# Optimization experiments

Hardware: AMD Instinct MI355X
Metric: run time of the kernel (lower is better)

The kernel has to match this reference:

```python
import jax, jax.numpy as jnp
import numpy as np

B, N, C, H, P = 4, 8192, 256, 4, 64  # batch, tokens(=input_size), hidden, heads, proj_size
D = C // H


def setup_inputs() -> dict:
    key = jax.random.key(0)
    ks = jax.random.split(key, 12)
    s = 1.0 / np.sqrt(C)
    inp = {
        "x": jax.random.normal(ks[0], (B, N, C), jnp.float32),
        "q": jax.random.normal(ks[1], (B, N, C), jnp.float32),
        "Wq": jax.random.normal(ks[2], (C, C), jnp.float32) * s,
        "Wk": jax.random.normal(ks[3], (C, C), jnp.float32) * s,
        "Wv_ca": jax.random.normal(ks[4], (C, C), jnp.float32) * s,
        "Wv_sa": jax.random.normal(ks[5], (C, C), jnp.float32) * s,
        "E_w": jax.random.normal(ks[6], (P, N), jnp.float32) * (1.0 / np.sqrt(N)),
        "E_b": jnp.zeros((P,), jnp.float32),
        "temp": jnp.ones((H, 1, 1), jnp.float32),
        "temp2": jnp.ones((H, 1, 1), jnp.float32),
        "Wo1": jax.random.normal(ks[7], (C // 2, C), jnp.float32) * s,
        "bo1": jnp.zeros((C // 2,), jnp.float32),
        "Wo2": jax.random.normal(ks[8], (C // 2, C), jnp.float32) * s,
        "bo2": jnp.zeros((C // 2,), jnp.float32),
    }
    return inp


def _l2norm(t):
    # F.normalize(dim=-1): x / max(||x||_2, 1e-12)
    n = jnp.sqrt(jnp.sum(t * t, axis=-1, keepdims=True))
    return t / jnp.maximum(n, 1e-12)


def reference(x, q, Wq, Wk, Wv_ca, Wv_sa, E_w, E_b, temp, temp2, Wo1, bo1, Wo2, bo2):
    b, n, c = x.shape
    h, d = H, c // H

    def split(t):  # [B,N,C] -> [B,H,d,N]
        return t.reshape(b, n, h, d).transpose(0, 2, 3, 1)

    qs = split(q @ Wq.T)
    ks = split(x @ Wk.T)
    v_ca = split(x @ Wv_ca.T)
    v_sa = split(x @ Wv_sa.T)

    # Linformer-style projections E (=F) over token dim N -> P
    k_proj = jnp.einsum('bhdn,pn->bhdp', ks, E_w) + E_b   # [B,H,d,P]
    v_proj = jnp.einsum('bhdn,pn->bhdp', v_sa, E_w) + E_b  # [B,H,d,P]

    qn = _l2norm(qs)
    kn = _l2norm(ks)

    # Channel attention: [B,H,d,d]
    attn_ca = jax.nn.softmax(jnp.einsum('bhdn,bhen->bhde', qn, kn) * temp, axis=-1)
    x_ca = jnp.einsum('bhde,bhen->bhdn', attn_ca, v_ca)
    x_ca = x_ca.transpose(0, 3, 1, 2).reshape(b, n, c)

    # Spatial (projected) attention: [B,H,N,P]
    attn_sa = jax.nn.softmax(jnp.einsum('bhdn,bhdp->bhnp', qn, k_proj) * temp2, axis=-1)
    x_sa = jnp.einsum('bhnp,bhdp->bhnd', attn_sa, v_proj)
    # faithful to original permute(0,3,1,2).reshape(B,N,C)
    x_sa = x_sa.transpose(0, 3, 1, 2).reshape(b, n, c)

    x_sa = x_sa @ Wo1.T + bo1
    x_ca = x_ca @ Wo2.T + bo2
    return jnp.concatenate((x_sa, x_ca), axis=-1)
```

## Files before the change

### kernel.cpp

```cpp
#include <hip/hip_runtime.h>
#include <hip/hip_bf16.h>

#define NN 8192
#define BNC 8388608

typedef unsigned short u16;
typedef unsigned int u32;
typedef __attribute__((ext_vector_type(8))) short bf16x8;
typedef __attribute__((ext_vector_type(4))) float f32x4;
typedef __attribute__((ext_vector_type(4))) float float4v;

__device__ __forceinline__ float bf2f(u16 u) {
    union { u32 i; float f; } c; c.i = ((u32)u) << 16; return c.f;
}
__device__ __forceinline__ u16 f2bf(float f) {
    union { float f; u32 i; } c; c.f = f;
    u32 x = c.i;
    u32 r = (x + 0x7fffu + ((x >> 16) & 1u)) >> 16;
    return (u16)r;
}
__device__ __forceinline__ void gl16(const u16* g, u16* l) {
    __builtin_amdgcn_global_load_lds(
        (const __attribute__((address_space(1))) void*)g,
        (__attribute__((address_space(3))) void*)l, 16, 0, 0);
}

__global__ void fill_kernel(float* __restrict__ out, float val) {
    int base = (blockIdx.x * 256 + threadIdx.x) * 4;
    #pragma unroll
    for (int i = 0; i < 4; ++i) out[base + i] = val;
}

__global__ void zeroconv_kernel(const float* __restrict__ q, const float* __restrict__ x,
                                const float* __restrict__ Wq, const float* __restrict__ Wk,
                                const float* __restrict__ Wo1, const float* __restrict__ Ew,
                                u16* __restrict__ qb, u16* __restrict__ xb,
                                u16* __restrict__ Wqb, u16* __restrict__ Wkb,
                                u16* __restrict__ Wo1b, u16* __restrict__ Ewb,
                                float* __restrict__ zbase) {
    if (blockIdx.x >= 8528) {
        int i = (blockIdx.x - 8528) * 256 + threadIdx.x;
        if (i < 67584) zbase[i] = 0.f;
        return;
    }
    size_t e = ((size_t)blockIdx.x * 256 + threadIdx.x) * 8;
    const float* src; u16* dst;
    if (e < 8388608)       { src = q   + e;              dst = qb   + e; }
    else if (e < 16777216) { src = x   + (e - 8388608);  dst = xb   + (e - 8388608); }
    else if (e < 16842752) { src = Wq  + (e - 16777216); dst = Wqb  + (e - 16777216); }
    else if (e < 16908288) { src = Wk  + (e - 16842752); dst = Wkb  + (e - 16842752); }
    else if (e < 16941056) { src = Wo1 + (e - 16908288); dst = Wo1b + (e - 16908288); }
    else                   { src = Ew  + (e - 16941056); dst = Ewb  + (e - 16941056); }
    float4v f0 = *(const float4v*)src, f1 = *(const float4v*)(src + 4);
    bf16x8 v;
    #pragma unroll
    for (int j = 0; j < 4; ++j) {
        v[j] = (short)f2bf(f0[j]); v[4 + j] = (short)f2bf(f1[j]);
    }
    *(bf16x8*)dst = v;
}

__global__ __launch_bounds__(256) void gemm_qkf(
    const u16* __restrict__ qb, const u16* __restrict__ xb,
    const u16* __restrict__ Wqb, const u16* __restrict__ Wkb,
    u16* __restrict__ Qb, u16* __restrict__ Kb,
    float* __restrict__ nq2, float* __restrict__ nk2)
{
    __shared__ u16 As[4096];
    __shared__ u16 Bs[4096];
    const int z = blockIdx.z;
    const u16* A = z ? xb : qb;
    const u16* Bt = z ? Wkb : Wqb;
    u16* O = z ? Kb : Qb;
    float* dstn = z ? nk2 : nq2;
    const int t = threadIdx.x, lane = t & 63, w = t >> 6;
    const int wr = w >> 1, wc = w & 1;
    const int fr = lane & 15, fk = (lane >> 4) * 8, r0 = (lane >> 4) * 4;
    const int m0 = blockIdx.x * 128, n0 = blockIdx.y * 128;
    const int b = m0 >> 13;
    const int row0 = t >> 2, k80 = (t & 3) * 8;
    const int row1 = (256 + t) >> 2, k81 = ((256 + t) & 3) * 8;

    f32x4 acc[4][4];
    #pragma unroll
    for (int i = 0; i < 4; ++i)
        #pragma unroll
        for (int j = 0; j < 4; ++j) acc[i][j] = (f32x4){0.f, 0.f, 0.f, 0.f};

    for (int kt = 0; kt < 8; ++kt) {
        const int k0 = kt * 32;
        gl16(A  + (size_t)(m0 + row0) * 256 + k0 + k80, &As[t * 8]);
        gl16(A  + (size_t)(m0 + row1) * 256 + k0 + k81, &As[(256 + t) * 8]);
        gl16(Bt + (size_t)(n0 + row0) * 256 + k0 + k80, &Bs[t * 8]);
        gl16(Bt + (size_t)(n0 + row1) * 256 + k0 + k81, &Bs[(256 + t) * 8]);
        __syncthreads();
        bf16x8 a[4], b[4];
        #pragma unroll
        for (int fm = 0; fm < 4; ++fm)
            a[fm] = *(const bf16x8*)&As[(wr * 64 + fm * 16 + fr) * 32 + fk];
        #pragma unroll
        for (int fn = 0; fn < 4; ++fn)
            b[fn] = *(const bf16x8*)&Bs[(wc * 64 + fn * 16 + fr) * 32 + fk];
        #pragma unroll
        for (int fm = 0; fm < 4; ++fm)
            #pragma unroll
            for (int fn = 0; fn < 4; ++fn)
                acc[fm][fn] = __builtin_amdgcn_mfma_f32_16x16x32_bf16(
                    a[fm], b[fn], acc[fm][fn], 0, 0, 0);
        __syncthreads();
    }

    #pragma unroll
    for (int fn = 0; fn < 4; ++fn) {
        int gcol = n0 + wc * 64 + fn * 16 + fr;
        float s = 0.f;
        #pragma unroll
        for (int fm = 0; fm < 4; ++fm) {
            #pragma unroll
            for (int r = 0; r < 4; ++r) {
                size_t grow = (size_t)(m0 + wr * 64 + fm * 16 + r0 + r);
                float v = acc[fm][fn][r];
                O[grow * 256 + gcol] = f2bf(v);
                s += v * v;
            }
        }
        s += __shfl_xor(s, 16);
        s += __shfl_xor(s, 32);
        if (lane < 16) atomicAdd(&dstn[b * 256 + gcol], s);
    }
}

__global__ __launch_bounds__(256) void xecalog_kernel(
    const u16* __restrict__ xb, const u16* __restrict__ Ewb, float* __restrict__ xE,
    const u16* __restrict__ Qb, const u16* __restrict__ Kb, float* __restrict__ cpart)
{
    __shared__ u16 smA[64][136];
    __shared__ u16 smB[64][136];
    const int t = threadIdx.x, lane = t & 63, w = t >> 6;
    const int fr = lane & 15, fk = (lane >> 4) * 8, r0 = (lane >> 4) * 4;

    f32x4 acc[4][4];
    #pragma unroll
    for (int i = 0; i < 4; ++i)
        #pragma unroll
        for (int j = 0; j < 4; ++j) acc[i][j] = (f32x4){0.f, 0.f, 0.f, 0.f};

    if (blockIdx.x < 128) {
        const int bkq = blockIdx.x >> 3, nc = blockIdx.x & 7;
        const int b = bkq >> 2, kq = bkq & 3;
        for (int it = 0; it < 8; ++it) {
            const int n0 = nc * 1024 + it * 128;
            #pragma unroll
            for (int i = 0; i < 4; ++i) {
                int c = i * 256 + t, tok = c >> 3, kl = (c & 7) * 8;
                const int sw = tok ^ ((kl >> 3) << 3);
                bf16x8 v = *(const bf16x8*)(xb + ((size_t)b * NN + n0 + tok) * 256 + kq * 64 + kl);
                #pragma unroll
                for (int j = 0; j < 8; ++j) smA[kl + j][sw] = (u16)v[j];
            }
            #pragma unroll
            for (int i = 0; i < 4; ++i) {
                int c = i * 256 + t, p = c >> 4, tk8 = (c & 15) * 8;
                *(bf16x8*)&smB[p][tk8] = *(const bf16x8*)(Ewb + (size_t)p * NN + n0 + tk8);
            }
            __syncthreads();
            bf16x8 a[4], bb[4];
            #pragma unroll
            for (int fm = 0; fm < 4; ++fm) {
                int row = fm * 16 + fr;
                a[fm] = *(const bf16x8*)&smA[row][(w * 32 + fk) ^ (((row >> 3) & 7) << 3)];
            }
            #pragma unroll
            for (int fn = 0; fn < 4; ++fn)
                bb[fn] = *(const bf16x8*)&smB[fn * 16 + fr][w * 32 + fk];
            #pragma unroll
            for (int fm = 0; fm < 4; ++fm)
                #pragma unroll
                for (int fn = 0; fn < 4; ++fn)
                    acc[fm][fn] = __builtin_amdgcn_mfma_f32_16x16x32_bf16(
                        a[fm], bb[fn], acc[fm][fn], 0, 0, 0);
            __syncthreads();
        }
        float* Cred = (float*)&smA[0][0];
        for (int ph = 0; ph < 4; ++ph) {
            if (w == ph) {
                #pragma unroll
                for (int fm = 0; fm < 4; ++fm)
                    #pragma unroll
                    for (int fn = 0; fn < 4; ++fn)
                        #pragma unroll
                        for (int r = 0; r < 4; ++r) {
                            int idx = (fm * 16 + r0 + r) * 64 + fn * 16 + fr;
                            if (ph == 0) Cred[idx] = acc[fm][fn][r];
                            else         Cred[idx] += acc[fm][fn][r];
                        }
            }
            __syncthreads();
        }
        float* dst = xE + (size_t)(b * 256 + kq * 64) * 64;
        #pragma unroll
        for (int i = 0; i < 16; ++i) atomicAdd(&dst[i * 256 + t], Cred[i * 256 + t]);
    } else {
        const int bx = blockIdx.x - 128;
        const int bh = bx >> 3, nc = bx & 7;
        const int b = bh >> 2, h = bh & 3;
        for (int it = 0; it < 8; ++it) {
            const int n0 = nc * 1024 + it * 128;
            #pragma unroll
            for (int i = 0; i < 4; ++i) {
                int c = i * 256 + t, tok = c >> 3, ch8 = (c & 7) * 8;
                const int sw = tok ^ ((ch8 >> 3) << 3);
                size_t g = ((size_t)b * NN + n0 + tok) * 256 + h * 64 + ch8;
                bf16x8 vq = *(const bf16x8*)(Qb + g);
                bf16x8 vk = *(const bf16x8*)(Kb + g);
                #pragma unroll
                for (int j = 0; j < 8; ++j) {
                    smA[ch8 + j][sw] = (u16)vq[j];
                    smB[ch8 + j][sw] = (u16)vk[j];
                }
            }
            __syncthreads();
            bf16x8 a[4], bb[4];
            #pragma unroll
            for (int fm = 0; fm < 4; ++fm) {
                int row = fm * 16 + fr;
                a[fm] = *(const bf16x8*)&smA[row][(w * 32 + fk) ^ (((row >> 3) & 7) << 3)];
            }
            #pragma unroll
            for (int fn = 0; fn < 4; ++fn) {
                int row = fn * 16 + fr;
                bb[fn] = *(const bf16x8*)&smB[row][(w * 32 + fk) ^ (((row >> 3) & 7) << 3)];
            }
            #pragma unroll
            for (int fm = 0; fm < 4; ++fm)
                #pragma unroll
                for (int fn = 0; fn < 4; ++fn)
                    acc[fm][fn] = __builtin_amdgcn_mfma_f32_16x16x32_bf16(
                        a[fm], bb[fn], acc[fm][fn], 0, 0, 0);
            __syncthreads();
        }
        float* Cred = (float*)&smA[0][0];
        for (int ph = 0; ph < 4; ++ph) {
            if (w == ph) {
                #pragma unroll
                for (int fm = 0; fm < 4; ++fm)
                    #pragma unroll
                    for (int fn = 0; fn < 4; ++fn)
                        #pragma unroll
                        for (int r = 0; r < 4; ++r) {
                            int idx = (fm * 16 + r0 + r) * 64 + fn * 16 + fr;
                            if (ph == 0) Cred[idx] = acc[fm][fn][r];
                            else         Cred[idx] += acc[fm][fn][r];
                        }
            }
            __syncthreads();
        }
        float* dst = cpart + (size_t)nc * 65536 + (size_t)bh * 4096;
        #pragma unroll
        for (int i = 0; i < 16; ++i) dst[i * 256 + t] = Cred[i * 256 + t];
    }
}

__global__ void smkv_kernel(const float* __restrict__ cpart, const float* __restrict__ nq2,
                            const float* __restrict__ nk2, const float* __restrict__ temp,
                            float* __restrict__ caprob,
                            const float* __restrict__ Wk, const float* __restrict__ Wvsa,
                            const float* __restrict__ xE, const float* __restrict__ Eb,
                            float* __restrict__ kp, float* __restrict__ vp) {
    if (blockIdx.x < 1024) {
        const int row = blockIdx.x;
        const int b = row >> 8, c = row & 255, h = c >> 6;
        const int e = threadIdx.x;
        const int i = row * 64 + e;
        float lg = cpart[i];
        #pragma unroll
        for (int nc = 1; nc < 8; ++nc) lg += cpart[(size_t)nc * 65536 + i];
        float nq = fmaxf(sqrtf(nq2[row]), 1e-12f);
        float nk = fmaxf(sqrtf(nk2[b * 256 + h * 64 + e]), 1e-12f);
        float v = lg / (nq * nk) * temp[h];
        __shared__ float red[64];
        red[e] = v; __syncthreads();
        for (int s = 32; s; s >>= 1) { if (e < s) red[e] = fmaxf(red[e], red[e + s]); __syncthreads(); }
        float m = red[0]; __syncthreads();
        float ex = __expf(v - m);
        red[e] = ex; __syncthreads();
        for (int s = 32; s; s >>= 1) { if (e < s) red[e] += red[e + s]; __syncthreads(); }
        caprob[i] = ex / red[0];
    } else {
        const int idx = blockIdx.x - 1024;
        const int z = idx >> 10, bc = idx & 1023;
        const int b = bc >> 8, c = bc & 255, p = threadIdx.x;
        const float* W = z ? Wvsa : Wk;
        float* dst = z ? vp : kp;
        float s = 0.f;
        for (int k = 0; k < 256; ++k)
            s += W[c * 256 + k] * xE[(size_t)(b * 256 + k) * 64 + p];
        dst[(size_t)(b * 256 + c) * 64 + p] = s + Eb[p];
    }
}

__global__ __launch_bounds__(256) void samw_kernel(
    const u16* __restrict__ Qb, const float* __restrict__ kp,
    const float* __restrict__ vp, const float* __restrict__ nq2,
    const float* __restrict__ temp2, u16* __restrict__ xsa,
    const float* __restrict__ caprob, const float* __restrict__ Wo2,
    const float* __restrict__ Wvca, u16* __restrict__ W2effb)
{
    __shared__ char smem[49152];
    const int t = threadIdx.x;
    if (blockIdx.x >= 512) {
        float* Ml = (float*)smem;
        const int bj = blockIdx.x - 512;
        const int b = bj >> 7, j = bj & 127;
        const int h = t >> 6, e = t & 63;
        float s = 0.f;
        #pragma unroll 8
        for (int d = 0; d < 64; ++d)
            s += Wo2[j * 256 + h * 64 + d] * caprob[(size_t)(b * 256 + h * 64 + d) * 64 + e];
        Ml[t] = s;
        __syncthreads();
        float s2 = 0.f;
        for (int c = 0; c < 256; ++c) s2 += Ml[c] * Wvca[c * 256 + t];
        W2effb[(size_t)bj * 256 + t] = f2bf(s2);
        return;
    }
    u16* Qs = (u16*)smem;
    u16* KT = (u16*)(smem + 32768);
    u16* VT = (u16*)(smem + 40960);
    const int nc = blockIdx.x & 31, bh = blockIdx.x >> 5, b = bh >> 2, h = bh & 3;
    const int lane = t & 63, w = t >> 6;
    const int fr = lane & 15, fk = (lane >> 4) * 8, r0 = (lane >> 4) * 4;

    #pragma unroll
    for (int i = 0; i < 8; ++i) {
        int c = i * 256 + t, tok = c >> 3, ch8 = (c & 7) * 8;
        *(bf16x8*)&Qs[c * 8] =
            *(const bf16x8*)(Qb + ((size_t)b * NN + nc * 256 + tok) * 256 + h * 64 + ch8);
    }
    {
        const int d = t >> 2, p0 = (t & 3) * 16;
        const float rqv = 1.0f / fmaxf(sqrtf(nq2[b * 256 + h * 64 + d]), 1e-12f);
        const float t2 = temp2[h];
        const float* kr = kp + (size_t)(b * 256 + h * 64 + d) * 64 + p0;
        #pragma unroll
        for (int j = 0; j < 16; ++j)
            KT[(p0 + j) * 64 + d] = f2bf(kr[j] * rqv * t2);
    }
    {
        const float* vs = vp + (size_t)(b * 256 + h * 64) * 64;
        #pragma unroll
        for (int i = 0; i < 2; ++i) {
            int c = i * 256 + t;
            bf16x8 v;
            #pragma unroll
            for (int j = 0; j < 8; ++j) v[j] = (short)f2bf(vs[c * 8 + j]);
            *(bf16x8*)&VT[c * 8] = v;
        }
    }
    __syncthreads();

    f32x4 acc[4][4];
    #pragma unroll
    for (int i = 0; i < 4; ++i)
        #pragma unroll
        for (int j = 0; j < 4; ++j) acc[i][j] = (f32x4){0.f, 0.f, 0.f, 0.f};
    #pragma unroll
    for (int ks = 0; ks < 2; ++ks) {
        bf16x8 a[4], bb[4];
        #pragma unroll
        for (int fm = 0; fm < 4; ++fm)
            a[fm] = *(const bf16x8*)&Qs[(w * 64 + fm * 16 + fr) * 64 + ks * 32 + fk];
        #pragma unroll
        for (int fn = 0; fn < 4; ++fn)
            bb[fn] = *(const bf16x8*)&KT[(fn * 16 + fr) * 64 + ks * 32 + fk];
        #pragma unroll
        for (int fm = 0; fm < 4; ++fm)
            #pragma unroll
            for (int fn = 0; fn < 4; ++fn)
                acc[fm][fn] = __builtin_amdgcn_mfma_f32_16x16x32_bf16(
                    a[fm], bb[fn], acc[fm][fn], 0, 0, 0);
    }
    __syncthreads();

    u16* Pw = Qs + w * 4096;
    #pragma unroll
    for (int fm = 0; fm < 4; ++fm) {
        #pragma unroll
        for (int r = 0; r < 4; ++r) {
            float m = fmaxf(fmaxf(acc[fm][0][r], acc[fm][1][r]),
                            fmaxf(acc[fm][2][r], acc[fm][3][r]));
            m = fmaxf(m, __shfl_xor(m, 1));
            m = fmaxf(m, __shfl_xor(m, 2));
            m = fmaxf(m, __shfl_xor(m, 4));
            m = fmaxf(m, __shfl_xor(m, 8));
            float e0 = __expf(acc[fm][0][r] - m), e1 = __expf(acc[fm][1][r] - m);
            float e2 = __expf(acc[fm][2][r] - m), e3 = __expf(acc[fm][3][r] - m);
            float s = e0 + e1 + e2 + e3;
            s += __shfl_xor(s, 1); s += __shfl_xor(s, 2);
            s += __shfl_xor(s, 4); s += __shfl_xor(s, 8);
            float rs = 1.0f / s;
            int row = fm * 16 + r0 + r;
            Pw[row * 64 +  0 + fr] = f2bf(e0 * rs);
            Pw[row * 64 + 16 + fr] = f2bf(e1 * rs);
            Pw[row * 64 + 32 + fr] = f2bf(e2 * rs);
            Pw[row * 64 + 48 + fr] = f2bf(e3 * rs);
        }
    }

    f32x4 acc2[4][4];
    #pragma unroll
    for (int i = 0; i < 4; ++i)
        #pragma unroll
        for (int j = 0; j < 4; ++j) acc2[i][j] = (f32x4){0.f, 0.f, 0.f, 0.f};
    #pragma unroll
    for (int ks = 0; ks < 2; ++ks) {
        bf16x8 a[4], bb[4];
        #pragma unroll
        for (int fm = 0; fm < 4; ++fm)
            a[fm] = *(const bf16x8*)&Pw[(fm * 16 + fr) * 64 + ks * 32 + fk];
        #pragma unroll
        for (int fn = 0; fn < 4; ++fn)
            bb[fn] = *(const bf16x8*)&VT[(fn * 16 + fr) * 64 + ks * 32 + fk];
        #pragma unroll
        for (int fm = 0; fm < 4; ++fm)
            #pragma unroll
            for (int fn = 0; fn < 4; ++fn)
                acc2[fm][fn] = __builtin_amdgcn_mfma_f32_16x16x32_bf16(
                    a[fm], bb[fn], acc2[fm][fn], 0, 0, 0);
    }
    __syncthreads();

    u16* X2 = Qs;
    #pragma unroll
    for (int fm = 0; fm < 4; ++fm)
        #pragma unroll
        for (int fn = 0; fn < 4; ++fn)
            #pragma unroll
            for (int r = 0; r < 4; ++r)
                X2[(w * 64 + fm * 16 + r0 + r) * 64 + fn * 16 + fr] = f2bf(acc2[fm][fn][r]);
    __syncthreads();

    {
        const int d = t >> 2, cq = (t & 3) * 64;
        u16* orow = xsa + ((size_t)b * NN + d * 128 + h * 32 + nc) * 256 + cq;
        #pragma unroll
        for (int i = 0; i < 8; ++i) {
            bf16x8 v;
            #pragma unroll
            for (int j = 0; j < 8; ++j) v[j] = (short)X2[(cq + i * 8 + j) * 64 + d];
            *(bf16x8*)&orow[i * 8] = v;
        }
    }
}

__global__ __launch_bounds__(256) void outgemm(
    const u16* __restrict__ xsa, const u16* __restrict__ xb,
    const u16* __restrict__ Wo1b, const u16* __restrict__ W2effb,
    const float* __restrict__ bo1, const float* __restrict__ bo2,
    float* __restrict__ out)
{
    __shared__ u16 As[4096];
    __shared__ u16 Bs[4096];
    const int z = blockIdx.z;
    const u16* A = z ? xb : xsa;
    const u16* Bt = z ? (W2effb + (size_t)(blockIdx.x >> 6) * 128 * 256) : Wo1b;
    const float* bias = z ? bo2 : bo1;
    const int outoff = z ? 128 : 0;
    const int t = threadIdx.x, lane = t & 63, w = t >> 6;
    const int wr = w >> 1, wc = w & 1;
    const int fr = lane & 15, fk = (lane >> 4) * 8, r0 = (lane >> 4) * 4;
    const int m0 = blockIdx.x * 128;
    const int row0 = t >> 2, k80 = (t & 3) * 8;
    const int row1 = (256 + t) >> 2, k81 = ((256 + t) & 3) * 8;

    f32x4 acc[4][4];
    #pragma unroll
    for (int i = 0; i < 4; ++i)
        #pragma unroll
        for (int j = 0; j < 4; ++j) acc[i][j] = (f32x4){0.f, 0.f, 0.f, 0.f};

    for (int kt = 0; kt < 8; ++kt) {
        const int k0 = kt * 32;
        gl16(A  + (size_t)(m0 + row0) * 256 + k0 + k80, &As[t * 8]);
        gl16(A  + (size_t)(m0 + row1) * 256 + k0 + k81, &As[(256 + t) * 8]);
        gl16(Bt + (size_t)row0 * 256 + k0 + k80, &Bs[t * 8]);
        gl16(Bt + (size_t)row1 * 256 + k0 + k81, &Bs[(256 + t) * 8]);
        __syncthreads();
        bf16x8 a[4], b[4];
        #pragma unroll
        for (int fm = 0; fm < 4; ++fm)
            a[fm] = *(const bf16x8*)&As[(wr * 64 + fm * 16 + fr) * 32 + fk];
        #pragma unroll
        for (int fn = 0; fn < 4; ++fn)
            b[fn] = *(const bf16x8*)&Bs[(wc * 64 + fn * 16 + fr) * 32 + fk];
        #pragma unroll
        for (int fm = 0; fm < 4; ++fm)
            #pragma unroll
            for (int fn = 0; fn < 4; ++fn)
                acc[fm][fn] = __builtin_amdgcn_mfma_f32_16x16x32_bf16(
                    a[fm], b[fn], acc[fm][fn], 0, 0, 0);
        __syncthreads();
    }

    #pragma unroll
    for (int fm = 0; fm < 4; ++fm)
        #pragma unroll
        for (int fn = 0; fn < 4; ++fn) {
            int gcol = wc * 64 + fn * 16 + fr;
            #pragma unroll
            for (int r = 0; r < 4; ++r) {
                size_t grow = (size_t)(m0 + wr * 64 + fm * 16 + r0 + r);
                out[grow * 256 + outoff + gcol] = acc[fm][fn][r] + bias[gcol];
            }
        }
}

extern "C" void kernel_launch(void* const* d_in, const int* in_sizes, int n_in,
                              void* d_out, int out_size, void* d_ws, size_t ws_size,
                              hipStream_t stream) {
    float* out = (float*)d_out;

    static const int expect[14] = {8388608, 8388608, 65536, 65536, 65536, 65536,
                                   524288, 64, 4, 4, 32768, 128, 32768, 128};
    bool ok = (n_in == 14) && (out_size == 8388608);
    if (ok) for (int i = 0; i < 14; ++i) ok = ok && (in_sizes[i] == expect[i]);
    if (!ok) {
        fill_kernel<<<dim3(8192), 256, 0, stream>>>(out, 3000.0f);
        return;
    }
    if (ws_size < 80000000u) {
        fill_kernel<<<dim3(8192), 256, 0, stream>>>(out, 1000.0f);
        return;
    }

    const float* x    = (const float*)d_in[0];
    const float* q    = (const float*)d_in[1];
    const float* Wq   = (const float*)d_in[2];
    const float* Wk   = (const float*)d_in[3];
    const float* Wvca = (const float*)d_in[4];
    const float* Wvsa = (const float*)d_in[5];
    const float* Ew   = (const float*)d_in[6];
    const float* Eb   = (const float*)d_in[7];
    const float* temp = (const float*)d_in[8];
    const float* temp2= (const float*)d_in[9];
    const float* Wo1  = (const float*)d_in[10];
    const float* bo1  = (const float*)d_in[11];
    const float* Wo2  = (const float*)d_in[12];
    const float* bo2  = (const float*)d_in[13];

    u16* Qb   = (u16*)d_ws;
    u16* Kb   = Qb + (size_t)BNC;
    u16* qb   = Kb + (size_t)BNC;
    u16* xb   = qb + (size_t)BNC;
    u16* Wqb  = xb + (size_t)BNC;
    u16* Wkb  = Wqb + 65536;
    u16* Wo1b = Wkb + 65536;
    u16* Ewb  = Wo1b + 32768;
    u16* W2effb = Ewb + 524288;
    u16* xsa  = Kb;
    float* fs    = (float*)(W2effb + 131072);
    float* nq2   = fs;
    float* nk2   = nq2 + 1024;
    float* xE    = nk2 + 1024;
    float* kp    = xE + 65536;
    float* vp    = kp + 65536;
    float* caprob= vp + 65536;
    float* cpart = caprob + 65536;

    zeroconv_kernel<<<dim3(8792), 256, 0, stream>>>(q, x, Wq, Wk, Wo1, Ew,
                                                    qb, xb, Wqb, Wkb, Wo1b, Ewb, nq2);
    gemm_qkf<<<dim3(256, 2, 2), 256, 0, stream>>>(qb, xb, Wqb, Wkb, Qb, Kb, nq2, nk2);
    xecalog_kernel<<<dim3(256), 256, 0, stream>>>(xb, Ewb, xE, Qb, Kb, cpart);
    smkv_kernel<<<dim3(3072), 64, 0, stream>>>(cpart, nq2, nk2, temp, caprob,
                                               Wk, Wvsa, xE, Eb, kp, vp);
    samw_kernel<<<dim3(1024), 256, 0, stream>>>(Qb, kp, vp, nq2, temp2, xsa,
                                                caprob, Wo2, Wvca, W2effb);
    outgemm<<<dim3(256, 1, 2), 256, 0, stream>>>(xsa, xb, Wo1b, W2effb, bo1, bo2, out);
}
```

Before: 110.3 us.

## Enlarge GEMM block tiles to 256 rows with 512 threads, async Q load

gemm_qkf and outgemm now run 512-thread blocks that each cover 256 rows instead of 128. The idea is to load each B (weight) tile once per 256 rows and halve the number of blocks. The samw kernel now loads its Q tile with async global-to-LDS loads instead of going through registers. The visible epilogue in gemm_qkf still indexes with wr=w>>1 and wc=w&1 for 8 waves, and its per-block norm reduction may not match the new tiling, so correctness is at risk.

```diff
diff --git a/kernel.cpp b/kernel.cpp
--- a/kernel.cpp
+++ b/kernel.cpp
@@ -60,13 +60,13 @@
     *(bf16x8*)dst = v;
 }
 
-__global__ __launch_bounds__(256) void gemm_qkf(
+__global__ __launch_bounds__(512) void gemm_qkf(
     const u16* __restrict__ qb, const u16* __restrict__ xb,
     const u16* __restrict__ Wqb, const u16* __restrict__ Wkb,
     u16* __restrict__ Qb, u16* __restrict__ Kb,
     float* __restrict__ nq2, float* __restrict__ nk2)
 {
-    __shared__ u16 As[4096];
+    __shared__ u16 As[8192];
     __shared__ u16 Bs[4096];
     const int z = blockIdx.z;
     const u16* A = z ? xb : qb;
@@ -76,10 +76,10 @@
     const int t = threadIdx.x, lane = t & 63, w = t >> 6;
     const int wr = w >> 1, wc = w & 1;
     const int fr = lane & 15, fk = (lane >> 4) * 8, r0 = (lane >> 4) * 4;
-    const int m0 = blockIdx.x * 128, n0 = blockIdx.y * 128;
+    const int m0 = blockIdx.x * 256, n0 = blockIdx.y * 128;
     const int b = m0 >> 13;
-    const int row0 = t >> 2, k80 = (t & 3) * 8;
-    const int row1 = (256 + t) >> 2, k81 = ((256 + t) & 3) * 8;
+    const int rA0 = t >> 2, kA0 = (t & 3) * 8;
+    const int rA1 = (512 + t) >> 2, kA1 = ((512 + t) & 3) * 8;
 
     f32x4 acc[4][4];
     #pragma unroll
@@ -89,24 +89,23 @@
 
     for (int kt = 0; kt < 8; ++kt) {
         const int k0 = kt * 32;
-        gl16(A  + (size_t)(m0 + row0) * 256 + k0 + k80, &As[t * 8]);
-        gl16(A  + (size_t)(m0 + row1) * 256 + k0 + k81, &As[(256 + t) * 8]);
-        gl16(Bt + (size_t)(n0 + row0) * 256 + k0 + k80, &Bs[t * 8]);
-        gl16(Bt + (size_t)(n0 + row1) * 256 + k0 + k81, &Bs[(256 + t) * 8]);
+        gl16(A  + (size_t)(m0 + rA0) * 256 + k0 + kA0, &As[t * 8]);
+        gl16(A  + (size_t)(m0 + rA1) * 256 + k0 + kA1, &As[(512 + t) * 8]);
+        gl16(Bt + (size_t)(n0 + rA0) * 256 + k0 + kA0, &Bs[t * 8]);
         __syncthreads();
-        bf16x8 a[4], b[4];
+        bf16x8 a[4], bfr[4];
         #pragma unroll
         for (int fm = 0; fm < 4; ++fm)
             a[fm] = *(const bf16x8*)&As[(wr * 64 + fm * 16 + fr) * 32 + fk];
         #pragma unroll
         for (int fn = 0; fn < 4; ++fn)
-            b[fn] = *(const bf16x8*)&Bs[(wc * 64 + fn * 16 + fr) * 32 + fk];
+            bfr[fn] = *(const bf16x8*)&Bs[(wc * 64 + fn * 16 + fr) * 32 + fk];
         #pragma unroll
         for (int fm = 0; fm < 4; ++fm)
             #pragma unroll
             for (int fn = 0; fn < 4; ++fn)
                 acc[fm][fn] = __builtin_amdgcn_mfma_f32_16x16x32_bf16(
-                    a[fm], b[fn], acc[fm][fn], 0, 0, 0);
+                    a[fm], bfr[fn], acc[fm][fn], 0, 0, 0);
         __syncthreads();
     }
 
@@ -334,8 +333,7 @@
     #pragma unroll
     for (int i = 0; i < 8; ++i) {
         int c = i * 256 + t, tok = c >> 3, ch8 = (c & 7) * 8;
-        *(bf16x8*)&Qs[c * 8] =
-            *(const bf16x8*)(Qb + ((size_t)b * NN + nc * 256 + tok) * 256 + h * 64 + ch8);
+        gl16(Qb + ((size_t)b * NN + nc * 256 + tok) * 256 + h * 64 + ch8, &Qs[c * 8]);
     }
     {
         const int d = t >> 2, p0 = (t & 3) * 16;
@@ -453,25 +451,25 @@
     }
 }
 
-__global__ __launch_bounds__(256) void outgemm(
+__global__ __launch_bounds__(512) void outgemm(
     const u16* __restrict__ xsa, const u16* __restrict__ xb,
     const u16* __restrict__ Wo1b, const u16* __restrict__ W2effb,
     const float* __restrict__ bo1, const float* __restrict__ bo2,
     float* __restrict__ out)
 {
-    __shared__ u16 As[4096];
+    __shared__ u16 As[8192];
     __shared__ u16 Bs[4096];
     const int z = blockIdx.z;
     const u16* A = z ? xb : xsa;
-    const u16* Bt = z ? (W2effb + (size_t)(blockIdx.x >> 6) * 128 * 256) : Wo1b;
+    const u16* Bt = z ? (W2effb + (size_t)(blockIdx.x >> 5) * 128 * 256) : Wo1b;
     const float* bias = z ? bo2 : bo1;
     const int outoff = z ? 128 : 0;
     const int t = threadIdx.x, lane = t & 63, w = t >> 6;
     const int wr = w >> 1, wc = w & 1;
     const int fr = lane & 15, fk = (lane >> 4) * 8, r0 = (lane >> 4) * 4;
-    const int m0 = blockIdx.x * 128;
-    const int row0 = t >> 2, k80 = (t & 3) * 8;
-    const int row1 = (256 + t) >> 2, k81 = ((256 + t) & 3) * 8;
+    const int m0 = blockIdx.x * 256;
+    const int rA0 = t >> 2, kA0 = (t & 3) * 8;
+    const int rA1 = (512 + t) >> 2, kA1 = ((512 + t) & 3) * 8;
 
     f32x4 acc[4][4];
     #pragma unroll
@@ -481,24 +479,23 @@
 
     for (int kt = 0; kt < 8; ++kt) {
         const int k0 = kt * 32;
-        gl16(A  + (size_t)(m0 + row0) * 256 + k0 + k80, &As[t * 8]);
-        gl16(A  + (size_t)(m0 + row1) * 256 + k0 + k81, &As[(256 + t) * 8]);
-        gl16(Bt + (size_t)row0 * 256 + k0 + k80, &Bs[t * 8]);
-        gl16(Bt + (size_t)row1 * 256 + k0 + k81, &Bs[(256 + t) * 8]);
+        gl16(A  + (size_t)(m0 + rA0) * 256 + k0 + kA0, &As[t * 8]);
+        gl16(A  + (size_t)(m0 + rA1) * 256 + k0 + kA1, &As[(512 + t) * 8]);
+        gl16(Bt + (size_t)rA0 * 256 + k0 + kA0, &Bs[t * 8]);
         __syncthreads();
-        bf16x8 a[4], b[4];
+        bf16x8 a[4], bfr[4];
         #pragma unroll
         for (int fm = 0; fm < 4; ++fm)
             a[fm] = *(const bf16x8*)&As[(wr * 64 + fm * 16 + fr) * 32 + fk];
         #pragma unroll
         for (int fn = 0; fn < 4; ++fn)
-            b[fn] = *(const bf16x8*)&Bs[(wc * 64 + fn * 16 + fr) * 32 + fk];
+            bfr[fn] = *(const bf16x8*)&Bs[(wc * 64 + fn * 16 + fr) * 32 + fk];
         #pragma unroll
         for (int fm = 0; fm < 4; ++fm)
             #pragma unroll
             for (int fn = 0; fn < 4; ++fn)
                 acc[fm][fn] = __builtin_amdgcn_mfma_f32_16x16x32_bf16(
-                    a[fm], b[fn], acc[fm][fn], 0, 0, 0);
+                    a[fm], bfr[fn], acc[fm][fn], 0, 0, 0);
         __syncthreads();
     }
 
@@ -569,11 +566,11 @@
 
     zeroconv_kernel<<<dim3(8792), 256, 0, stream>>>(q, x, Wq, Wk, Wo1, Ew,
                                                     qb, xb, Wqb, Wkb, Wo1b, Ewb, nq2);
-    gemm_qkf<<<dim3(256, 2, 2), 256, 0, stream>>>(qb, xb, Wqb, Wkb, Qb, Kb, nq2, nk2);
+    gemm_qkf<<<dim3(128, 2, 2), 512, 0, stream>>>(qb, xb, Wqb, Wkb, Qb, Kb, nq2, nk2);
     xecalog_kernel<<<dim3(256), 256, 0, stream>>>(xb, Ewb, xE, Qb, Kb, cpart);
     smkv_kernel<<<dim3(3072), 64, 0, stream>>>(cpart, nq2, nk2, temp, caprob,
                                                Wk, Wvsa, xE, Eb, kp, vp);
     samw_kernel<<<dim3(1024), 256, 0, stream>>>(Qb, kp, vp, nq2, temp2, xsa,
                                                 caprob, Wo2, Wvca, W2effb);
-    outgemm<<<dim3(256, 1, 2), 256, 0, stream>>>(xsa, xb, Wo1b, W2effb, bo1, bo2, out);
-}
+    outgemm<<<dim3(128, 1, 2), 512, 0, stream>>>(xsa, xb, Wo1b, W2effb, bo1, bo2, out);
+}
```

Measured after the change: 116.4 us. +5.6%, slower.
